# Optimization experiments

Hardware: AMD Instinct MI355X
Metric: run time of the kernel (lower is better)

## Reference

```python
import jax, jax.numpy as jnp
import numpy as np

N_NODES = 100000
N_EDGES = 600000
D = 128


def setup_inputs() -> dict:
    key = jax.random.key(0)
    ks = jax.random.split(key, 12)
    inp = {
        'feat': jax.random.normal(ks[0], (N_NODES, D), dtype=jnp.float32),
        'W_tran': jax.random.normal(ks[1], (D, D), dtype=jnp.float32) * (1.0 / np.sqrt(D)),
        'att_w1': jax.random.normal(ks[2], (4 * D, D), dtype=jnp.float32) * (1.0 / np.sqrt(D)),
        'att_b1': jax.random.normal(ks[3], (4 * D,), dtype=jnp.float32) * 0.01,
        'att_w2': jax.random.normal(ks[4], (1, 4 * D), dtype=jnp.float32) * (1.0 / np.sqrt(4 * D)),
        'trans_w': jax.random.uniform(ks[5], (N_EDGES,), dtype=jnp.float32),
        'geo_src': jax.random.randint(ks[6], (N_EDGES,), 0, N_NODES, dtype=jnp.int32),
        'geo_dst': jax.random.randint(ks[7], (N_EDGES,), 0, N_NODES, dtype=jnp.int32),
        'cat_src': jax.random.randint(ks[8], (N_EDGES,), 0, N_NODES, dtype=jnp.int32),
        'cat_dst': jax.random.randint(ks[9], (N_EDGES,), 0, N_NODES, dtype=jnp.int32),
        'trans_src': jax.random.randint(ks[10], (N_EDGES,), 0, N_NODES, dtype=jnp.int32),
        'trans_dst': jax.random.randint(ks[11], (N_EDGES,), 0, N_NODES, dtype=jnp.int32),
    }
    return inp


def _mean_agg(f, src, dst, n):
    # copy_u('f','m') then mean('m', .) : gather src feats, segment-mean by dst
    msum = jax.ops.segment_sum(f[src], dst, num_segments=n)
    cnt = jax.ops.segment_sum(jnp.ones((src.shape[0],), f.dtype), dst, num_segments=n)
    return msum / jnp.maximum(cnt, 1.0)[:, None]


def reference(feat, W_tran, att_w1, att_b1, att_w2, trans_w,
              geo_src, geo_dst, cat_src, cat_dst, trans_src, trans_dst):
    n = feat.shape[0]
    # feat_tran: Linear(D, D, bias=False) -> x @ W^T
    f = feat @ W_tran.T
    geo = _mean_agg(f, geo_src, geo_dst, n)            # [N, D]
    cat = _mean_agg(f, cat_src, cat_dst, n)            # [N, D]
    # u_mul_e('f','w') then sum: weighted gather + segment-sum by dst
    trans = jax.ops.segment_sum(f[trans_src] * trans_w[:, None], trans_dst, num_segments=n)
    z = jnp.stack([geo, trans, cat], axis=1)           # [N, 3, D]
    # SemanticAttention: Linear -> tanh -> Linear(no bias), mean over nodes, softmax over relations
    h = jnp.tanh(jnp.einsum('nrd,hd->nrh', z, att_w1) + att_b1)   # [N, 3, 4D]
    w = jnp.einsum('nrh,oh->nro', h, att_w2).mean(0)              # [3, 1]
    beta = jax.nn.softmax(w, axis=0)                              # [3, 1]
    fused = (beta[None, :, :] * z).sum(1)                         # [N, D]
    return jax.nn.leaky_relu(fused, negative_slope=0.2)
```

## Files before the change

kernel.cpp:

```cpp
#include <hip/hip_runtime.h>
#include <math.h>

#define DD 128
#define NNODES 100000
#define NEDGES 600000
#define NREL 3
#define MTOT (NREL*NNODES)
#define NTILES (NNODES/16)
#define RT_PER_BLK 8
#define NBLK_REL ((NTILES + RT_PER_BLK - 1)/RT_PER_BLK)
#define ATT_WAVES 8

#define BSHIFT 9
#define NBUCK ((NNODES + 511) >> BSHIFT)
#define GBUCK (NREL*NBUCK)
#define CAP 4096
#define CAPH 2048
#define P1_THREADS 512
#define P1_EPT 8
#define P1_EPB (P1_THREADS*P1_EPT)
#define P1_BLOCKS ((NREL*NEDGES + P1_EPB - 1)/P1_EPB)

#define TR_BLOCKS ((NTILES + 7)/8)
#define CVT_BLOCKS ((512*DD/4 + 511)/512)
#define FRONT_BLOCKS (P1_BLOCKS + TR_BLOCKS + CVT_BLOCKS)

typedef __attribute__((ext_vector_type(8))) short short8;
typedef __attribute__((ext_vector_type(4))) float f32x4;

__device__ inline float bf2f(unsigned short u){ return __uint_as_float(((unsigned int)u)<<16); }
__device__ inline float bflo(unsigned int u){ return __uint_as_float(u<<16); }
__device__ inline float bfhi(unsigned int u){ return __uint_as_float(u & 0xffff0000u); }
__device__ inline unsigned short f2bf(float f){
    unsigned int i = __float_as_uint(f);
    unsigned int r = (i + 0x7fffu + ((i>>16)&1u)) >> 16;
    return (unsigned short)r;
}
__device__ inline unsigned int pack2(float lo, float hi){
    return (unsigned int)f2bf(lo) | ((unsigned int)f2bf(hi) << 16);
}
__device__ inline short8 cvt8(const float* __restrict__ p){
    f32x4 a = *(const f32x4*)p;
    f32x4 b = *(const f32x4*)(p+4);
    short8 t;
    t[0]=(short)f2bf(a[0]); t[1]=(short)f2bf(a[1]); t[2]=(short)f2bf(a[2]); t[3]=(short)f2bf(a[3]);
    t[4]=(short)f2bf(b[0]); t[5]=(short)f2bf(b[1]); t[6]=(short)f2bf(b[2]); t[7]=(short)f2bf(b[3]);
    return t;
}
__device__ inline void acc8(float* a, float w, uint4 v){
    a[0] += w*bflo(v.x); a[1] += w*bfhi(v.x);
    a[2] += w*bflo(v.y); a[3] += w*bfhi(v.y);
    a[4] += w*bflo(v.z); a[5] += w*bfhi(v.z);
    a[6] += w*bflo(v.w); a[7] += w*bfhi(v.w);
}

__global__ __launch_bounds__(512) void k_front(
    const float* __restrict__ feat, const float* __restrict__ W,
    const float* __restrict__ aw1,
    const int* __restrict__ s0, const int* __restrict__ d0,
    const int* __restrict__ s1, const int* __restrict__ d1,
    const int* __restrict__ s2, const int* __restrict__ d2,
    const float* __restrict__ tw,
    int* __restrict__ bcur, int2* __restrict__ slab, float* __restrict__ wslab,
    unsigned short* __restrict__ w1_bf, unsigned short* __restrict__ f_out)
{
    __shared__ char smraw[32768];
    int bid = blockIdx.x;

    if (bid < P1_BLOCKS){
        int* hist = (int*)smraw;
        for (int i=threadIdx.x; i<GBUCK; i+=512) hist[i]=0;
        __syncthreads();

        int e0 = bid * P1_EPB;
        int ss[P1_EPT], dd_[P1_EPT], gb[P1_EPT]; float wv[P1_EPT];
        #pragma unroll
        for (int j=0;j<P1_EPT;++j){
            int e = e0 + j*512 + threadIdx.x;
            gb[j] = -1;
            if (e < NREL*NEDGES){
                int rel = e / NEDGES; int i = e - rel*NEDGES;
                const int* s = (rel==0)?s0:(rel==1)?s1:s2;
                const int* d = (rel==0)?d0:(rel==1)?d1:d2;
                ss[j]=s[i]; dd_[j]=d[i];
                wv[j] = (rel==2)? tw[i] : 0.f;
                gb[j] = rel*NBUCK + (dd_[j]>>BSHIFT);
                atomicAdd(&hist[gb[j]], 1);
            }
        }
        __syncthreads();
        for (int i=threadIdx.x; i<GBUCK; i+=512){
            int c = hist[i];
            hist[i] = (c>0) ? atomicAdd(&bcur[i], c) : 0;
        }
        __syncthreads();
        #pragma unroll
        for (int j=0;j<P1_EPT;++j){
            if (gb[j] >= 0){
                int off = atomicAdd(&hist[gb[j]], 1);
                int2 pr; pr.x = ss[j]; pr.y = dd_[j];
                slab[(size_t)gb[j]*CAP + off] = pr;
                if (gb[j] >= 2*NBUCK) wslab[(size_t)(gb[j]-2*NBUCK)*CAP + off] = wv[j];
            }
        }
    } else if (bid < P1_BLOCKS + TR_BLOCKS){
        short8* wlds = (short8*)smraw;
        {
            int t = threadIdx.x;
            int row = t >> 2;
            int c0  = (t & 3) * 4;
            const float* wrow = W + (size_t)row*DD;
            #pragma unroll
            for (int cc=0; cc<4; ++cc){
                int chunk = c0 + cc;
                wlds[row*16 + (chunk ^ (row & 7))] = cvt8(wrow + chunk*8);
            }
        }
        __syncthreads();

        int wid = (bid - P1_BLOCKS)*8 + (threadIdx.x>>6);
        if (wid >= NTILES) return;
        int lane = threadIdx.x & 63;
        int m = lane & 15, quad = lane >> 4;
        int n0 = wid*16;

        short8 a[4];
        const float* arow = feat + (size_t)(n0+m)*DD;
        #pragma unroll
        for (int ks=0; ks<4; ++ks) a[ks] = cvt8(arow + ks*32 + quad*8);

        #pragma unroll
        for (int ct=0; ct<8; ++ct){
            f32x4 acc = {0.f,0.f,0.f,0.f};
            int brow = ct*16 + m;
            #pragma unroll
            for (int ks=0; ks<4; ++ks){
                short8 b = wlds[brow*16 + ((ks*4 + quad) ^ (brow & 7))];
                acc = __builtin_amdgcn_mfma_f32_16x16x32_bf16(a[ks], b, acc, 0,0,0);
            }
            int col = ct*16 + m;
            #pragma unroll
            for (int i=0;i<4;++i)
                f_out[(size_t)(n0+quad*4+i)*DD + col] = f2bf(acc[i]);
        }
    } else {
        int gid = (bid - P1_BLOCKS - TR_BLOCKS)*512 + threadIdx.x;
        if (gid < 512*DD/4){
            f32x4 v = ((const f32x4*)aw1)[gid];
            ushort4 o;
            o.x=f2bf(v[0]); o.y=f2bf(v[1]); o.z=f2bf(v[2]); o.w=f2bf(v[3]);
            ((ushort4*)w1_bf)[gid] = o;
        }
    }
}

__global__ __launch_bounds__(512) void k_csragg(
    const int2* __restrict__ slab, const float* __restrict__ wslab,
    const int* __restrict__ bcur,
    const unsigned short* __restrict__ f,
    unsigned short* __restrict__ z)
{
    __shared__ int lcnt[256];
    __shared__ int lsc[256];
    __shared__ int psum[256];
    __shared__ int es_l[CAPH];
    __shared__ float ewt_l[CAPH];

    int gb2 = blockIdx.x;
    int rel = gb2 / (2*NBUCK);
    int rem = gb2 - rel*2*NBUCK;
    int b = rem >> 1, half = rem & 1;
    int hn0 = (b << BSHIFT) + half*256;
    if (hn0 >= NNODES) return;
    int nn = min(256, NNODES - hn0);
    int gb = rel*NBUCK + b;
    int ecount = bcur[gb];
    const int2* ep = slab + (size_t)gb*CAP;
    int t = threadIdx.x;
    bool wr = (rel == 2);

    if (t < 256) lcnt[t] = 0;
    __syncthreads();
    for (int i=t; i<ecount; i+=512){
        unsigned lo = (unsigned)(ep[i].y - hn0);
        if (lo < 256u) atomicAdd(&lcnt[lo], 1);
    }
    __syncthreads();
    int v = 0;
    if (t < 256){ v = lcnt[t]; psum[t] = v; }
    __syncthreads();
    for (int off=1; off<256; off<<=1){
        int x = 0;
        if (t < 256 && t >= off) x = psum[t-off];
        __syncthreads();
        if (t < 256) psum[t] += x;
        __syncthreads();
    }
    if (t < 256) lsc[t] = psum[t] - v;
    __syncthreads();
    for (int i=t; i<ecount; i+=512){
        int2 pr = ep[i];
        unsigned lo = (unsigned)(pr.y - hn0);
        if (lo < 256u){
            int pos = atomicAdd(&lsc[lo], 1);
            es_l[pos] = pr.x;
            if (wr) ewt_l[pos] = wslab[(size_t)b*CAP + i];
        }
    }
    __syncthreads();

    int grp = t >> 4, c = t & 15;
    for (int pass=0; pass<8; ++pass){
        int n = pass*32 + grp;
        if (n >= nn) break;
        int deg = lcnt[n];
        int start = lsc[n] - deg;
        float a[8] = {0,0,0,0,0,0,0,0};
        int i = 0;
        if (!wr){
            for (; i+3 < deg; i += 4){
                int s0 = es_l[start+i],   s1 = es_l[start+i+1];
                int s2 = es_l[start+i+2], s3 = es_l[start+i+3];
                uint4 v0 = *(const uint4*)(f + (size_t)s0*DD + c*8);
                uint4 v1 = *(const uint4*)(f + (size_t)s1*DD + c*8);
                uint4 v2 = *(const uint4*)(f + (size_t)s2*DD + c*8);
                uint4 v3 = *(const uint4*)(f + (size_t)s3*DD + c*8);
                acc8(a,1.f,v0); acc8(a,1.f,v1); acc8(a,1.f,v2); acc8(a,1.f,v3);
            }
            if (i+1 < deg){
                int s0 = es_l[start+i], s1 = es_l[start+i+1];
                uint4 v0 = *(const uint4*)(f + (size_t)s0*DD + c*8);
                uint4 v1 = *(const uint4*)(f + (size_t)s1*DD + c*8);
                acc8(a,1.f,v0); acc8(a,1.f,v1);
                i += 2;
            }
            if (i < deg){
                int s = es_l[start+i];
                uint4 vv = *(const uint4*)(f + (size_t)s*DD + c*8);
                acc8(a,1.f,vv);
            }
            float sc = 1.f/fmaxf((float)deg, 1.f);
            #pragma unroll
            for (int k=0;k<8;++k) a[k] *= sc;
        } else {
            for (; i+3 < deg; i += 4){
                int s0 = es_l[start+i],   s1 = es_l[start+i+1];
                int s2 = es_l[start+i+2], s3 = es_l[start+i+3];
                float w0 = ewt_l[start+i],   w1 = ewt_l[start+i+1];
                float w2 = ewt_l[start+i+2], w3 = ewt_l[start+i+3];
                uint4 v0 = *(const uint4*)(f + (size_t)s0*DD + c*8);
                uint4 v1 = *(const uint4*)(f + (size_t)s1*DD + c*8);
                uint4 v2 = *(const uint4*)(f + (size_t)s2*DD + c*8);
                uint4 v3 = *(const uint4*)(f + (size_t)s3*DD + c*8);
                acc8(a,w0,v0); acc8(a,w1,v1); acc8(a,w2,v2); acc8(a,w3,v3);
            }
            if (i+1 < deg){
                int s0 = es_l[start+i], s1 = es_l[start+i+1];
                float w0 = ewt_l[start+i], w1 = ewt_l[start+i+1];
                uint4 v0 = *(const uint4*)(f + (size_t)s0*DD + c*8);
                uint4 v1 = *(const uint4*)(f + (size_t)s1*DD + c*8);
                acc8(a,w0,v0); acc8(a,w1,v1);
                i += 2;
            }
            if (i < deg){
                int s = es_l[start+i];
                float w = ewt_l[start+i];
                uint4 vv = *(const uint4*)(f + (size_t)s*DD + c*8);
                acc8(a,w,vv);
            }
        }
        uint4 o;
        o.x = pack2(a[0], a[1]);
        o.y = pack2(a[2], a[3]);
        o.z = pack2(a[4], a[5]);
        o.w = pack2(a[6], a[7]);
        *(uint4*)(z + (size_t)(rel*NNODES + hn0 + n)*DD + c*8) = o;
    }
}

__global__ __launch_bounds__(512, 4) void k_att(
    const unsigned short* __restrict__ z,
    const unsigned short* __restrict__ w1,
    const float* __restrict__ bias1,
    const float* __restrict__ wv2,
    float* __restrict__ w_part)
{
    __shared__ uint4 sm[RT_PER_BLK*256];
    __shared__ float sred[ATT_WAVES];
    const float C2 = 2.8853900817779268f;

    int rel = blockIdx.x / NBLK_REL;
    int nb  = blockIdx.x % NBLK_REL;
    int trt0 = nb * RT_PER_BLK;
    int rt_count = min(RT_PER_BLK, NTILES - trt0);
    int row0 = trt0 * 16;
    const unsigned short* zrel = z + (size_t)rel*NNODES*DD;

    int lane = threadIdx.x & 63;
    int wv   = threadIdx.x >> 6;
    int m = lane & 15, quad = lane >> 4;

    short8 bq[16];
    float ww[4], bbc[4];
    #pragma unroll
    for (int ct=0; ct<4; ++ct){
        int col = (wv*4 + ct)*16 + m;
        const short8* brow = (const short8*)(w1 + (size_t)col*DD);
        #pragma unroll
        for (int ks=0; ks<4; ++ks) bq[ct*4+ks] = brow[ks*4 + quad];
        ww[ct]  = wv2[col];
        bbc[ct] = bias1[col] * C2;
    }

    int valid_rows = rt_count * 16;
    #pragma unroll
    for (int i=0; i<4; ++i){
        int u = i*512 + threadIdx.x;
        int row = u >> 4, kc = u & 15;
        if (row < valid_rows){
            uint4 v = *(const uint4*)(zrel + (size_t)(row0+row)*DD + kc*8);
            int rt = row >> 4, mm = row & 15;
            sm[rt*256 + kc*16 + (mm ^ kc)] = v;
        }
    }
    __syncthreads();

    const short8* smx = (const short8*)sm;
    int o0 = (0  + quad)*16 + (m ^ (0  + quad));
    int o1 = (4  + quad)*16 + (m ^ (4  + quad));
    int o2 = (8  + quad)*16 + (m ^ (8  + quad));
    int o3 = (12 + quad)*16 + (m ^ (12 + quad));

    float s_r[4] = {0.f,0.f,0.f,0.f};
    short8 a0 = smx[o0], a1 = smx[o1], a2 = smx[o2], a3 = smx[o3];
    for (int rt=0; rt<rt_count; ++rt){
        short8 n0_, n1_, n2_, n3_;
        if (rt+1 < rt_count){
            int nbse = (rt+1)*256;
            n0_ = smx[nbse + o0];
            n1_ = smx[nbse + o1];
            n2_ = smx[nbse + o2];
            n3_ = smx[nbse + o3];
        } else { n0_ = a0; n1_ = a1; n2_ = a2; n3_ = a3; }
        #pragma unroll
        for (int ct=0; ct<4; ++ct){
            f32x4 acc = {0.f,0.f,0.f,0.f};
            acc = __builtin_amdgcn_mfma_f32_16x16x32_bf16(a0, bq[ct*4+0], acc, 0,0,0);
            acc = __builtin_amdgcn_mfma_f32_16x16x32_bf16(a1, bq[ct*4+1], acc, 0,0,0);
            acc = __builtin_amdgcn_mfma_f32_16x16x32_bf16(a2, bq[ct*4+2], acc, 0,0,0);
            acc = __builtin_amdgcn_mfma_f32_16x16x32_bf16(a3, bq[ct*4+3], acc, 0,0,0);
            #pragma unroll
            for (int i=0;i<4;++i){
                float e = __builtin_amdgcn_exp2f(__builtin_fmaf(acc[i], C2, bbc[ct]));
                s_r[ct] += __builtin_amdgcn_rcpf(e + 1.f);
            }
        }
        a0 = n0_; a1 = n1_; a2 = n2_; a3 = n3_;
    }
    float s_all = 0.f;
    #pragma unroll
    for (int ct=0; ct<4; ++ct)
        s_all += ww[ct]*(float)(4*rt_count) - 2.f*ww[ct]*s_r[ct];
    #pragma unroll
    for (int off=32; off; off>>=1) s_all += __shfl_xor(s_all, off);
    if (lane == 0) sred[wv] = s_all;
    __syncthreads();
    if (threadIdx.x == 0){
        float tt = 0.f;
        #pragma unroll
        for (int i=0;i<ATT_WAVES;++i) tt += sred[i];
        atomicAdd(&w_part[rel*8 + (nb & 7)], tt);
    }
}

__global__ __launch_bounds__(256) void k_final(
    const unsigned short* __restrict__ z0, const unsigned short* __restrict__ z1,
    const unsigned short* __restrict__ z2,
    const float* __restrict__ w_part, float* __restrict__ out)
{
    int gid = blockIdx.x*256 + threadIdx.x;
    if (gid >= NNODES*DD/4) return;
    const float invN = 1.f / (float)NNODES;
    float w0=0.f, w1=0.f, w2=0.f;
    #pragma unroll
    for (int i=0;i<8;++i){ w0 += w_part[i]; w1 += w_part[8+i]; w2 += w_part[16+i]; }
    w0 *= invN; w1 *= invN; w2 *= invN;
    float mx = fmaxf(w0, fmaxf(w1, w2));
    const float LOG2E = 1.4426950408889634f;
    float e0 = __builtin_amdgcn_exp2f((w0-mx)*LOG2E);
    float e1 = __builtin_amdgcn_exp2f((w1-mx)*LOG2E);
    float e2 = __builtin_amdgcn_exp2f((w2-mx)*LOG2E);
    float inv = 1.f/(e0+e1+e2);
    float b0 = e0*inv, b1 = e1*inv, b2 = e2*inv;
    ushort4 g = ((const ushort4*)z0)[gid];
    ushort4 t = ((const ushort4*)z1)[gid];
    ushort4 c = ((const ushort4*)z2)[gid];
    f32x4 o;
    float gv[4] = {bf2f(g.x),bf2f(g.y),bf2f(g.z),bf2f(g.w)};
    float tv[4] = {bf2f(t.x),bf2f(t.y),bf2f(t.z),bf2f(t.w)};
    float cv[4] = {bf2f(c.x),bf2f(c.y),bf2f(c.z),bf2f(c.w)};
    #pragma unroll
    for (int i=0;i<4;++i){
        float x = b0*gv[i] + b1*tv[i] + b2*cv[i];
        o[i] = (x > 0.f) ? x : 0.2f*x;
    }
    ((f32x4*)out)[gid] = o;
}

extern "C" void kernel_launch(void* const* d_in, const int* in_sizes, int n_in,
                              void* d_out, int out_size, void* d_ws, size_t ws_size,
                              hipStream_t stream)
{
    const float* feat = (const float*)d_in[0];
    const float* W    = (const float*)d_in[1];
    const float* aw1  = (const float*)d_in[2];
    const float* ab1  = (const float*)d_in[3];
    const float* aw2  = (const float*)d_in[4];
    const float* tw   = (const float*)d_in[5];
    const int* geo_src   = (const int*)d_in[6];
    const int* geo_dst   = (const int*)d_in[7];
    const int* cat_src   = (const int*)d_in[8];
    const int* cat_dst   = (const int*)d_in[9];
    const int* trans_src = (const int*)d_in[10];
    const int* trans_dst = (const int*)d_in[11];

    char* ws = (char*)d_ws;
    float* w_part = (float*)ws;
    int*   bcur   = (int*)(w_part + 64);
    unsigned short* w1_bf = (unsigned short*)(bcur + 640);
    unsigned short* z = w1_bf + 512*DD;

    unsigned short* f_bf = (unsigned short*)d_out;
    int2*  slab  = (int2*)((char*)d_out + (size_t)NNODES*DD*sizeof(unsigned short));
    float* wslab = (float*)(slab + (size_t)GBUCK*CAP);

    (void)hipMemsetAsync(w_part, 0, (64 + 640)*sizeof(int), stream);

    k_front<<<FRONT_BLOCKS, 512, 0, stream>>>(feat, W, aw1,
                                              geo_src, geo_dst, cat_src, cat_dst,
                                              trans_src, trans_dst, tw,
                                              bcur, slab, wslab, w1_bf, f_bf);

    k_csragg<<<NREL*2*NBUCK, 512, 0, stream>>>(slab, wslab, bcur, f_bf, z);

    k_att<<<NREL*NBLK_REL, 512, 0, stream>>>(z, w1_bf, ab1, aw2, w_part);

    unsigned short* z_geo   = z;
    unsigned short* z_cat   = z + (size_t)NNODES*DD;
    unsigned short* z_trans = z + (size_t)2*NNODES*DD;
    int dg = (NNODES*DD/4 + 255)/256;
    k_final<<<dg, 256, 0, stream>>>(z_geo, z_cat, z_trans, w_part, (float*)d_out);
}
```

Before: 324.0 us.

## Use 256-node buckets in aggregation and read attention inputs directly from global

Dst buckets shrink from 512 to 256 nodes with half the slab capacity, so each aggregation block owns one bucket and no longer scans and filters edges belonging to the other half. Separately, the attention kernel drops its LDS staging of z tiles and loads MFMA A-operands straight from global memory with register prefetch. The bucket change halves per-bucket capacity, which risks overflow if a 256-node bucket receives more than 2048 edges. Removing LDS staging trades the shared-memory copy and barrier for less coalesced global loads.

After: 358.8 us. 1.11x slower.

```diff
diff --git a/kernel.cpp b/kernel.cpp
--- a/kernel.cpp
+++ b/kernel.cpp
@@ -11,11 +11,10 @@
 #define NBLK_REL ((NTILES + RT_PER_BLK - 1)/RT_PER_BLK)
 #define ATT_WAVES 8
 
-#define BSHIFT 9
-#define NBUCK ((NNODES + 511) >> BSHIFT)
+#define BSHIFT 8
+#define NBUCK ((NNODES + 255) >> BSHIFT)
 #define GBUCK (NREL*NBUCK)
-#define CAP 4096
-#define CAPH 2048
+#define CAP 2048
 #define P1_THREADS 512
 #define P1_EPT 8
 #define P1_EPB (P1_THREADS*P1_EPT)
@@ -163,17 +162,13 @@
     __shared__ int lcnt[256];
     __shared__ int lsc[256];
     __shared__ int psum[256];
-    __shared__ int es_l[CAPH];
-    __shared__ float ewt_l[CAPH];
-
-    int gb2 = blockIdx.x;
-    int rel = gb2 / (2*NBUCK);
-    int rem = gb2 - rel*2*NBUCK;
-    int b = rem >> 1, half = rem & 1;
-    int hn0 = (b << BSHIFT) + half*256;
-    if (hn0 >= NNODES) return;
-    int nn = min(256, NNODES - hn0);
-    int gb = rel*NBUCK + b;
+    __shared__ int es_l[CAP];
+    __shared__ float ewt_l[CAP];
+
+    int gb = blockIdx.x;
+    int rel = gb / NBUCK, b = gb - rel*NBUCK;
+    int n0 = b << BSHIFT;
+    int nn = min(256, NNODES - n0);
     int ecount = bcur[gb];
     const int2* ep = slab + (size_t)gb*CAP;
     int t = threadIdx.x;
@@ -181,10 +176,8 @@
 
     if (t < 256) lcnt[t] = 0;
     __syncthreads();
-    for (int i=t; i<ecount; i+=512){
-        unsigned lo = (unsigned)(ep[i].y - hn0);
-        if (lo < 256u) atomicAdd(&lcnt[lo], 1);
-    }
+    for (int i=t; i<ecount; i+=512)
+        atomicAdd(&lcnt[ep[i].y - n0], 1);
     __syncthreads();
     int v = 0;
     if (t < 256){ v = lcnt[t]; psum[t] = v; }
@@ -200,12 +193,9 @@
     __syncthreads();
     for (int i=t; i<ecount; i+=512){
         int2 pr = ep[i];
-        unsigned lo = (unsigned)(pr.y - hn0);
-        if (lo < 256u){
-            int pos = atomicAdd(&lsc[lo], 1);
-            es_l[pos] = pr.x;
-            if (wr) ewt_l[pos] = wslab[(size_t)b*CAP + i];
-        }
+        int pos = atomicAdd(&lsc[pr.y - n0], 1);
+        es_l[pos] = pr.x;
+        if (wr) ewt_l[pos] = wslab[(size_t)b*CAP + i];
     }
     __syncthreads();
 
@@ -274,7 +264,7 @@
         o.y = pack2(a[2], a[3]);
         o.z = pack2(a[4], a[5]);
         o.w = pack2(a[6], a[7]);
-        *(uint4*)(z + (size_t)(rel*NNODES + hn0 + n)*DD + c*8) = o;
+        *(uint4*)(z + (size_t)(rel*NNODES + n0 + n)*DD + c*8) = o;
     }
 }
 
@@ -285,7 +275,6 @@
     const float* __restrict__ wv2,
     float* __restrict__ w_part)
 {
-    __shared__ uint4 sm[RT_PER_BLK*256];
     __shared__ float sred[ATT_WAVES];
     const float C2 = 2.8853900817779268f;
 
@@ -312,35 +301,21 @@
         bbc[ct] = bias1[col] * C2;
     }
 
-    int valid_rows = rt_count * 16;
-    #pragma unroll
-    for (int i=0; i<4; ++i){
-        int u = i*512 + threadIdx.x;
-        int row = u >> 4, kc = u & 15;
-        if (row < valid_rows){
-            uint4 v = *(const uint4*)(zrel + (size_t)(row0+row)*DD + kc*8);
-            int rt = row >> 4, mm = row & 15;
-            sm[rt*256 + kc*16 + (mm ^ kc)] = v;
-        }
-    }
-    __syncthreads();
-
-    const short8* smx = (const short8*)sm;
-    int o0 = (0  + quad)*16 + (m ^ (0  + quad));
-    int o1 = (4  + quad)*16 + (m ^ (4  + quad));
-    int o2 = (8  + quad)*16 + (m ^ (8  + quad));
-    int o3 = (12 + quad)*16 + (m ^ (12 + quad));
+    const unsigned short* rp = zrel + (size_t)(row0 + m)*DD + quad*8;
 
     float s_r[4] = {0.f,0.f,0.f,0.f};
-    short8 a0 = smx[o0], a1 = smx[o1], a2 = smx[o2], a3 = smx[o3];
+    short8 a0 = *(const short8*)(rp);
+    short8 a1 = *(const short8*)(rp + 32);
+    short8 a2 = *(const short8*)(rp + 64);
+    short8 a3 = *(const short8*)(rp + 96);
     for (int rt=0; rt<rt_count; ++rt){
         short8 n0_, n1_, n2_, n3_;
         if (rt+1 < rt_count){
-            int nbse = (rt+1)*256;
-            n0_ = smx[nbse + o0];
-            n1_ = smx[nbse + o1];
-            n2_ = smx[nbse + o2];
-            n3_ = smx[nbse + o3];
+            const unsigned short* np = rp + (size_t)(rt+1)*16*DD;
+            n0_ = *(const short8*)(np);
+            n1_ = *(const short8*)(np + 32);
+            n2_ = *(const short8*)(np + 64);
+            n3_ = *(const short8*)(np + 96);
         } else { n0_ = a0; n1_ = a1; n2_ = a2; n3_ = a3; }
         #pragma unroll
         for (int ct=0; ct<4; ++ct){
@@ -427,21 +402,21 @@
     char* ws = (char*)d_ws;
     float* w_part = (float*)ws;
     int*   bcur   = (int*)(w_part + 64);
-    unsigned short* w1_bf = (unsigned short*)(bcur + 640);
+    unsigned short* w1_bf = (unsigned short*)(bcur + 1280);
     unsigned short* z = w1_bf + 512*DD;
 
     unsigned short* f_bf = (unsigned short*)d_out;
     int2*  slab  = (int2*)((char*)d_out + (size_t)NNODES*DD*sizeof(unsigned short));
     float* wslab = (float*)(slab + (size_t)GBUCK*CAP);
 
-    (void)hipMemsetAsync(w_part, 0, (64 + 640)*sizeof(int), stream);
+    (void)hipMemsetAsync(w_part, 0, (64 + 1280)*sizeof(int), stream);
 
     k_front<<<FRONT_BLOCKS, 512, 0, stream>>>(feat, W, aw1,
                                               geo_src, geo_dst, cat_src, cat_dst,
                                               trans_src, trans_dst, tw,
                                               bcur, slab, wslab, w1_bf, f_bf);
 
-    k_csragg<<<NREL*2*NBUCK, 512, 0, stream>>>(slab, wslab, bcur, f_bf, z);
+    k_csragg<<<GBUCK, 512, 0, stream>>>(slab, wslab, bcur, f_bf, z);
 
     k_att<<<NREL*NBLK_REL, 512, 0, stream>>>(z, w1_bf, ab1, aw2, w_part);
 
```
